# Optimization experiments

Measured on AMD Instinct MI355X. Metric: run time of the kernel, lower is better.

## Reference

```python
import jax, jax.numpy as jnp
import numpy as np

N_NODES = 100000
N_EDGES = 1600000
IN_DIM = 128
HID = 128
NUM_LAYERS = 3


def _sage_conv(h, src, dst, Wl, Wr, b, n_nodes):
    # PyG SAGEConv (aggr='mean'): out = lin_l(mean_j x_j) + lin_r(x_i)
    agg = jax.ops.segment_sum(h[src], dst, num_segments=n_nodes)
    cnt = jax.ops.segment_sum(jnp.ones((src.shape[0],), dtype=h.dtype), dst,
                              num_segments=n_nodes)
    mean = agg / jnp.maximum(cnt, 1.0)[:, None]
    return mean @ Wl + h @ Wr + b


def setup_inputs() -> dict:
    key = jax.random.key(0)
    ks = jax.random.split(key, 16)
    x = jax.random.normal(ks[0], (N_NODES, IN_DIM), dtype=jnp.float32)
    edge_index = jax.random.randint(ks[1], (2, N_EDGES), 0, N_NODES, dtype=jnp.int32)
    reranker_scores = jax.random.normal(ks[2], (N_NODES,), dtype=jnp.float32)
    inp = {"x": x, "edge_index": edge_index, "reranker_scores": reranker_scores}
    dims = [IN_DIM, HID, HID]
    for i in range(NUM_LAYERS):
        d_in = dims[i]
        s = 1.0 / np.sqrt(d_in)
        inp[f"Wl{i}"] = jax.random.uniform(ks[3 + 3 * i], (d_in, HID), jnp.float32, -s, s)
        inp[f"Wr{i}"] = jax.random.uniform(ks[4 + 3 * i], (d_in, HID), jnp.float32, -s, s)
        inp[f"b{i}"] = jax.random.uniform(ks[5 + 3 * i], (HID,), jnp.float32, -s, s)
    sh = 1.0 / np.sqrt(HID * NUM_LAYERS)
    inp["Ws"] = jax.random.uniform(ks[12], (HID * NUM_LAYERS, 1), jnp.float32, -sh, sh)
    inp["bs"] = jax.random.uniform(ks[13], (1,), jnp.float32, -sh, sh)
    inp["alpha"] = jnp.asarray(0.65, dtype=jnp.float32)
    return inp


def reference(x, edge_index, reranker_scores,
              Wl0, Wr0, b0, Wl1, Wr1, b1, Wl2, Wr2, b2,
              Ws, bs, alpha):
    src, dst = edge_index[0], edge_index[1]
    n = x.shape[0]
    params = [(Wl0, Wr0, b0), (Wl1, Wr1, b1), (Wl2, Wr2, b2)]
    xs = []
    h = x
    for (Wl, Wr, b) in params:
        h = jax.nn.relu(_sage_conv(h, src, dst, Wl, Wr, b, n))
        # dropout: eval-mode identity
        xs.append(h)
    hj = jnp.concatenate(xs, axis=-1)                 # [N, HID*NUM_LAYERS]
    gnn_scores = (hj @ Ws + bs)[:, 0]                 # [N]
    a = jax.nn.sigmoid(alpha)
    return a * reranker_scores + (1.0 - a) * gnn_scores
```

## Files before the change

### kernel.cpp

```cpp
#include <hip/hip_runtime.h>
#include <hip/hip_bf16.h>
#include <cstdint>

#define N_NODES 100000
#define HID 128
#define NBINS 391
#define CHUNK 4096

typedef __attribute__((ext_vector_type(8))) short short8v;
typedef __attribute__((ext_vector_type(4))) float floatx4;

__device__ __forceinline__ float bflo(unsigned v) { return __uint_as_float(v << 16); }
__device__ __forceinline__ float bfhi(unsigned v) { return __uint_as_float(v & 0xffff0000u); }
__device__ __forceinline__ unsigned short f2bf(float f) {
    unsigned u = __float_as_uint(f);
    unsigned r = (u + 0x7fffu + ((u >> 16) & 1u)) >> 16;
    return (unsigned short)r;
}

__global__ __launch_bounds__(256) void prep_kernel(const float* __restrict__ x,
                                                   unsigned short* __restrict__ xb, int total8,
                                                   const float* __restrict__ Wl0, const float* __restrict__ Wr0,
                                                   const float* __restrict__ Wl1, const float* __restrict__ Wr1,
                                                   const float* __restrict__ Wl2, const float* __restrict__ Wr2,
                                                   unsigned short* __restrict__ Bp) {
    if ((int)blockIdx.x < total8 / 256) {
        int i = blockIdx.x * 256 + threadIdx.x;
        const float4* p = (const float4*)x + (size_t)i * 2;
        float4 a = p[0], b = p[1];
        uint4 o;
        o.x = f2bf(a.x) | ((unsigned)f2bf(a.y) << 16);
        o.y = f2bf(a.z) | ((unsigned)f2bf(a.w) << 16);
        o.z = f2bf(b.x) | ((unsigned)f2bf(b.y) << 16);
        o.w = f2bf(b.z) | ((unsigned)f2bf(b.w) << 16);
        *(uint4*)(xb + (size_t)i * 8) = o;
    } else {
        int idx = ((int)blockIdx.x - total8 / 256) * 256 + threadIdx.x;
        if (idx >= 12288) return;
        int g = idx & 3, c = (idx >> 2) & 127, s = (idx >> 9) & 3, t = (idx >> 11) & 1, L = idx >> 12;
        const float* W = (t == 0) ? (L == 0 ? Wl0 : (L == 1 ? Wl1 : Wl2))
                                  : (L == 0 ? Wr0 : (L == 1 ? Wr1 : Wr2));
        int k0 = s * 32 + g * 8;
        uint4 o;
        o.x = f2bf(W[(k0 + 0) * 128 + c]) | ((unsigned)f2bf(W[(k0 + 1) * 128 + c]) << 16);
        o.y = f2bf(W[(k0 + 2) * 128 + c]) | ((unsigned)f2bf(W[(k0 + 3) * 128 + c]) << 16);
        o.z = f2bf(W[(k0 + 4) * 128 + c]) | ((unsigned)f2bf(W[(k0 + 5) * 128 + c]) << 16);
        o.w = f2bf(W[(k0 + 6) * 128 + c]) | ((unsigned)f2bf(W[(k0 + 7) * 128 + c]) << 16);
        size_t chunk = (((size_t)(L * 2 + t) * 4 + s) * 128 + c) * 4 + g;
        *(uint4*)(Bp + chunk * 8) = o;
    }
}


__global__ __launch_bounds__(256) void binhist_kernel(const int* __restrict__ dst,
                                                      int* __restrict__ cntMat, int E) {
    __shared__ int lcnt[512];
    const int tid = threadIdx.x;
    lcnt[tid] = 0; lcnt[tid + 256] = 0;
    __syncthreads();
    int base = blockIdx.x * CHUNK;
    int end = base + CHUNK; if (end > E) end = E;
    for (int i = base + tid; i < end; i += 256) atomicAdd(&lcnt[dst[i] >> 8], 1);
    __syncthreads();
    for (int j = tid; j < NBINS; j += 256) cntMat[(size_t)blockIdx.x * NBINS + j] = lcnt[j];
}

__global__ __launch_bounds__(512) void colscan_kernel(int* __restrict__ cntMat,
                                                      int* __restrict__ binCnt, int nch) {
    __shared__ int wsum[8];
    const int j = blockIdx.x;
    const int tid = threadIdx.x;
    const int lane = tid & 63, w = tid >> 6;
    int v = (tid < nch) ? cntMat[(size_t)tid * NBINS + j] : 0;
    int s = v;
    #pragma unroll
    for (int o = 1; o < 64; o <<= 1) {
        int t = __shfl_up(s, o, 64);
        if (lane >= o) s += t;
    }
    if (lane == 63) wsum[w] = s;
    __syncthreads();
    if (w == 0 && lane < 8) {
        int t = wsum[lane];
        int ss = t;
        #pragma unroll
        for (int o = 1; o < 8; o <<= 1) {
            int u = __shfl_up(ss, o, 64);
            if (lane >= o) ss += u;
        }
        wsum[lane] = ss - t;
    }
    __syncthreads();
    int excl = (s - v) + wsum[w];
    if (tid < nch) cntMat[(size_t)tid * NBINS + j] = excl;
    if (tid == 511) binCnt[j] = excl + v;
}

__global__ __launch_bounds__(512) void binbase_kernel(const int* __restrict__ binCnt,
                                                      int* __restrict__ binBase,
                                                      int* __restrict__ offs, int E) {
    __shared__ int wsum[8];
    const int tid = threadIdx.x;
    const int lane = tid & 63, w = tid >> 6;
    int v = (tid < NBINS) ? binCnt[tid] : 0;
    int s = v;
    #pragma unroll
    for (int o = 1; o < 64; o <<= 1) {
        int t = __shfl_up(s, o, 64);
        if (lane >= o) s += t;
    }
    if (lane == 63) wsum[w] = s;
    __syncthreads();
    if (w == 0 && lane < 8) {
        int t = wsum[lane];
        int ss = t;
        #pragma unroll
        for (int o = 1; o < 8; o <<= 1) {
            int u = __shfl_up(ss, o, 64);
            if (lane >= o) ss += u;
        }
        wsum[lane] = ss - t;
    }
    __syncthreads();
    if (tid < NBINS) binBase[tid] = (s - v) + wsum[w];
    if (tid == 0) offs[N_NODES] = E;
}

__global__ __launch_bounds__(256) void binscat_kernel(const int* __restrict__ src, const int* __restrict__ dst,
                                                      const int* __restrict__ cntMat,
                                                      const int* __restrict__ binBase,
                                                      unsigned* __restrict__ binned, int E) {
    __shared__ int cur[512];
    const int tid = threadIdx.x;
    const int row = blockIdx.x;
    for (int j = tid; j < NBINS; j += 256) cur[j] = cntMat[(size_t)row * NBINS + j] + binBase[j];
    __syncthreads();
    int base = row * CHUNK;
    int end = base + CHUNK; if (end > E) end = E;
    for (int i = base + tid; i < end; i += 256) {
        int d = dst[i];
        int s = src[i];
        int bin = d >> 8;
        int pos = atomicAdd(&cur[bin], 1);
        binned[pos] = (unsigned)s | ((unsigned)(d & 255) << 20);
    }
}

__global__ __launch_bounds__(256) void bincsr_kernel(const unsigned* __restrict__ binned,
                                                     const int* __restrict__ binBase, const int* __restrict__ binCnt,
                                                     int* __restrict__ esrc, int* __restrict__ offs) {
    __shared__ int h[256];
    __shared__ int cur[256];
    __shared__ int ssrc[8192];
    const int tid = threadIdx.x;
    const int bin = blockIdx.x;
    const int base = binBase[bin];
    const int cnt = binCnt[bin];
    h[tid] = 0;
    __syncthreads();
    for (int i = tid; i < cnt; i += 256) atomicAdd(&h[binned[base + i] >> 20], 1);
    __syncthreads();
    int v = h[tid];
    for (int o = 1; o < 256; o <<= 1) {
        int t = (tid >= o) ? h[tid - o] : 0;
        __syncthreads();
        h[tid] += t;
        __syncthreads();
    }
    int excl = h[tid] - v;
    cur[tid] = excl;
    int node = (bin << 8) + tid;
    if (node < N_NODES) offs[node] = base + excl;
    __syncthreads();
    for (int i = tid; i < cnt; i += 256) {
        unsigned p = binned[base + i];
        int pos = atomicAdd(&cur[p >> 20], 1);
        int s = (int)(p & 0xFFFFFu);
        if (pos < 8192) ssrc[pos] = s;
        else esrc[base + pos] = s;
    }
    __syncthreads();
    int lim = cnt < 8192 ? cnt : 8192;
    for (int i = tid; i < lim; i += 256) esrc[base + i] = ssrc[i];
}

__global__ __launch_bounds__(256) void agg_kernel(const unsigned short* __restrict__ h,
                                                  const int* __restrict__ offs,
                                                  const int* __restrict__ esrc,
                                                  unsigned short* __restrict__ mean) {
    const int lane = threadIdx.x & 63;
    const int node = blockIdx.x * 4 + (threadIdx.x >> 6);
    const int half = lane >> 5;
    const int fl = lane & 31;
    const int beg = offs[node], end = offs[node + 1];
    const int nb = end - beg;
    float a0 = 0.f, a1 = 0.f, a2 = 0.f, a3 = 0.f;
    for (int base = 0; base < nb; base += 64) {
        int m = nb - base; if (m > 64) m = 64;
        int sv = (lane < m) ? esrc[beg + base + lane] : 0;
        int j = 0;
        for (; j + 16 <= m; j += 16) {
            uint2 v[8];
            #pragma unroll
            for (int p = 0; p < 8; ++p) {
                int s = __shfl(sv, j + 2 * p + half, 64);
                v[p] = *(const uint2*)(h + (size_t)s * HID + fl * 4);
            }
            #pragma unroll
            for (int p = 0; p < 8; ++p) {
                a0 += bflo(v[p].x); a1 += bfhi(v[p].x);
                a2 += bflo(v[p].y); a3 += bfhi(v[p].y);
            }
        }
        for (; j + 2 <= m; j += 2) {
            int s = __shfl(sv, j + half, 64);
            uint2 vv = *(const uint2*)(h + (size_t)s * HID + fl * 4);
            a0 += bflo(vv.x); a1 += bfhi(vv.x);
            a2 += bflo(vv.y); a3 += bfhi(vv.y);
        }
        if (j < m) {
            int s = __shfl(sv, j, 64);
            if (half == 0) {
                uint2 vv = *(const uint2*)(h + (size_t)s * HID + fl * 4);
                a0 += bflo(vv.x); a1 += bfhi(vv.x);
                a2 += bflo(vv.y); a3 += bfhi(vv.y);
            }
        }
    }
    a0 += __shfl_xor(a0, 32, 64);
    a1 += __shfl_xor(a1, 32, 64);
    a2 += __shfl_xor(a2, 32, 64);
    a3 += __shfl_xor(a3, 32, 64);
    if (half == 0) {
        float inv = 1.f / (float)(nb > 0 ? nb : 1);
        uint2 o;
        o.x = (unsigned)f2bf(a0 * inv) | ((unsigned)f2bf(a1 * inv) << 16);
        o.y = (unsigned)f2bf(a2 * inv) | ((unsigned)f2bf(a3 * inv) << 16);
        *(uint2*)(mean + (size_t)node * HID + fl * 4) = o;
    }
}

__global__ __launch_bounds__(256) void gemm_kernel(const unsigned short* __restrict__ Am,
                                                   const unsigned short* __restrict__ Ah,
                                                   const unsigned short* __restrict__ Bp,
                                                   const float* __restrict__ bias,
                                                   const float* __restrict__ Wsl,
                                                   unsigned short* __restrict__ hout,
                                                   float* __restrict__ score,
                                                   const float* __restrict__ rrs,
                                                   const float* __restrict__ bsp,
                                                   const float* __restrict__ alphap,
                                                   float* __restrict__ outF,
                                                   const int accum, const int writeH, const int doFinal) {
    __shared__ unsigned short At[2 * 64 * 128];
    __shared__ float sred[2][64];
    const int tid = threadIdx.x;
    const int lane = tid & 63;
    const int w = tid >> 6;
    const int wm = w & 1, wn = w >> 1;
    const int rowBase = blockIdx.x * 64;
    const int halfRow = lane & 15;
    const int g = lane >> 4;

    {
        const unsigned short* srcs[2] = { Am, Ah };
        #pragma unroll
        for (int r = 0; r < 8; ++r) {
            int c = r * 256 + tid;
            int sIdx = c >> 10;
            int rem = c & 1023;
            int row = rem >> 4, slot = rem & 15;
            int gslot = slot ^ (row & 15);
            int grow = rowBase + row; if (grow >= N_NODES) grow = N_NODES - 1;
            const unsigned short* gp = srcs[sIdx] + (size_t)grow * HID + gslot * 8;
            unsigned ldsOff = (unsigned)(r * 4096 + w * 1024);
            __builtin_amdgcn_global_load_lds((const __attribute__((address_space(1))) void*)gp,
                                             (__attribute__((address_space(3))) void*)((char*)At + ldsOff),
                                             16, 0, 0);
        }
    }
    __syncthreads();

    floatx4 acc[2][4];
    #pragma unroll
    for (int m = 0; m < 2; m++)
        #pragma unroll
        for (int n = 0; n < 4; n++) acc[m][n] = (floatx4){0.f, 0.f, 0.f, 0.f};

    #pragma unroll
    for (int t = 0; t < 2; t++) {
        #pragma unroll
        for (int s = 0; s < 4; s++) {
            int slot = (s * 4 + g) ^ halfRow;
            int row0 = wm * 32 + halfRow;
            short8v a0 = *(const short8v*)&At[t * 8192 + row0 * 128 + slot * 8];
            short8v a1 = *(const short8v*)&At[t * 8192 + (row0 + 16) * 128 + slot * 8];
            #pragma unroll
            for (int n = 0; n < 4; n++) {
                int col = wn * 64 + n * 16 + halfRow;
                short8v b = *(const short8v*)&Bp[((((size_t)(t * 4 + s)) * 128 + col) * 4 + g) * 8];
                acc[0][n] = __builtin_amdgcn_mfma_f32_16x16x32_bf16(a0, b, acc[0][n], 0, 0, 0);
                acc[1][n] = __builtin_amdgcn_mfma_f32_16x16x32_bf16(a1, b, acc[1][n], 0, 0, 0);
            }
        }
    }

    #pragma unroll
    for (int m = 0; m < 2; m++) {
        #pragma unroll
        for (int i = 0; i < 4; i++) {
            int rloc = wm * 32 + m * 16 + g * 4 + i;
            int grow = rowBase + rloc;
            float ps = 0.f;
            #pragma unroll
            for (int n = 0; n < 4; n++) {
                int col = wn * 64 + n * 16 + halfRow;
                float v = acc[m][n][i] + bias[col];
                v = fmaxf(v, 0.f);
                if (writeH && grow < N_NODES) hout[(size_t)grow * HID + col] = f2bf(v);
                ps += v * Wsl[col];
            }
            ps += __shfl_xor(ps, 1, 64);
            ps += __shfl_xor(ps, 2, 64);
            ps += __shfl_xor(ps, 4, 64);
            ps += __shfl_xor(ps, 8, 64);
            if (halfRow == 0) sred[wn][rloc] = ps;
        }
    }
    __syncthreads();
    if (w == 0) {
        int grow = rowBase + lane;
        if (grow < N_NODES) {
            float tot = sred[0][lane] + sred[1][lane];
            if (doFinal) {
                float sc = score[grow] + tot;
                float a = 1.f / (1.f + __expf(-alphap[0]));
                outF[grow] = a * rrs[grow] + (1.f - a) * (sc + bsp[0]);
            } else {
                score[grow] = accum ? (score[grow] + tot) : tot;
            }
        }
    }
}

extern "C" void kernel_launch(void* const* d_in, const int* in_sizes, int n_in,
                              void* d_out, int out_size, void* d_ws, size_t ws_size,
                              hipStream_t stream) {
    const float* x     = (const float*)d_in[0];
    const int*   eidx  = (const int*)d_in[1];
    const float* rrs   = (const float*)d_in[2];
    const float* Wl0   = (const float*)d_in[3];
    const float* Wr0   = (const float*)d_in[4];
    const float* b0    = (const float*)d_in[5];
    const float* Wl1   = (const float*)d_in[6];
    const float* Wr1   = (const float*)d_in[7];
    const float* b1    = (const float*)d_in[8];
    const float* Wl2   = (const float*)d_in[9];
    const float* Wr2   = (const float*)d_in[10];
    const float* b2    = (const float*)d_in[11];
    const float* Ws    = (const float*)d_in[12];
    const float* bs    = (const float*)d_in[13];
    const float* alpha = (const float*)d_in[14];

    const int N = N_NODES;
    const int E = in_sizes[1] / 2;
    const int* src = eidx;
    const int* dst = eidx + E;

    uintptr_t p = (uintptr_t)d_ws;
    auto alloc = [&](size_t bytes) -> void* {
        p = (p + 255) & ~(uintptr_t)255;
        void* r = (void*)p;
        p += bytes;
        return r;
    };
    int*            offs    = (int*)alloc((size_t)(N + 1) * 4);
    int*            esrc    = (int*)alloc((size_t)E * 4);
    float*          score   = (float*)alloc((size_t)N * 4);
    int*            binBase = (int*)alloc(512 * 4);
    int*            binCnt  = (int*)alloc(512 * 4);
    unsigned short* xb      = (unsigned short*)alloc((size_t)N * HID * 2);
    unsigned short* bufA    = (unsigned short*)alloc((size_t)N * HID * 2);
    unsigned short* bufB    = (unsigned short*)alloc((size_t)N * HID * 2);
    unsigned short* Bp      = (unsigned short*)alloc((size_t)3 * 32768 * 2);

    int*      cntMat = (int*)bufA;
    unsigned* binned = (unsigned*)bufB;

    const int nch = (E + CHUNK - 1) / CHUNK;

    prep_kernel<<<N * HID / 8 / 256 + 48, 256, 0, stream>>>(x, xb, N * HID / 8,
                                                            Wl0, Wr0, Wl1, Wr1, Wl2, Wr2, Bp);

    binhist_kernel<<<nch, 256, 0, stream>>>(dst, cntMat, E);
    colscan_kernel<<<NBINS, 512, 0, stream>>>(cntMat, binCnt, nch);
    binbase_kernel<<<1, 512, 0, stream>>>(binCnt, binBase, offs, E);
    binscat_kernel<<<nch, 256, 0, stream>>>(src, dst, cntMat, binBase, binned, E);
    bincsr_kernel<<<NBINS, 256, 0, stream>>>(binned, binBase, binCnt, esrc, offs);

    const int aggGrid  = N / 4;
    const int gemmGrid = (N + 63) / 64;
    float* outF = (float*)d_out;

    agg_kernel<<<aggGrid, 256, 0, stream>>>(xb, offs, esrc, bufA);
    gemm_kernel<<<gemmGrid, 256, 0, stream>>>(bufA, xb, Bp + 0 * 32768, b0, Ws + 0 * HID, bufA, score,
                                              rrs, bs, alpha, outF, 0, 1, 0);
    agg_kernel<<<aggGrid, 256, 0, stream>>>(bufA, offs, esrc, bufB);
    gemm_kernel<<<gemmGrid, 256, 0, stream>>>(bufB, bufA, Bp + 1 * 32768, b1, Ws + 1 * HID, bufB, score,
                                              rrs, bs, alpha, outF, 1, 1, 0);
    agg_kernel<<<aggGrid, 256, 0, stream>>>(bufB, offs, esrc, bufA);
    gemm_kernel<<<gemmGrid, 256, 0, stream>>>(bufA, bufB, Bp + 2 * 32768, b2, Ws + 2 * HID, bufA, score,
                                              rrs, bs, alpha, outF, 1, 0, 1);
}
```

Baseline: 318.0 us.

## Fuse neighbor mean aggregation into the per-layer GEMM kernel via LDS

Merges the separate aggregation and GEMM kernels into one kernel per layer. Each block gathers the mean of neighbour features for its 64 rows straight into swizzled shared memory while the self features stream in asynchronously, then runs the MFMA GEMM. This removes writing and re-reading the intermediate mean buffer and cuts the launches from six to three. In exchange, grid parallelism for the gather drops (1563 blocks of 64 nodes instead of 25000 blocks of 4), and each wave processes 16 nodes one after another, which may reduce latency hiding.

Result: slower. 401.7 us (+26.3%).

```diff
diff --git a/kernel.cpp b/kernel.cpp
--- a/kernel.cpp
+++ b/kernel.cpp
@@ -184,102 +184,100 @@
     for (int i = tid; i < lim; i += 256) esrc[base + i] = ssrc[i];
 }
 
-__global__ __launch_bounds__(256) void agg_kernel(const unsigned short* __restrict__ h,
-                                                  const int* __restrict__ offs,
-                                                  const int* __restrict__ esrc,
-                                                  unsigned short* __restrict__ mean) {
-    const int lane = threadIdx.x & 63;
-    const int node = blockIdx.x * 4 + (threadIdx.x >> 6);
+__global__ __launch_bounds__(256) void fused_kernel(const unsigned short* __restrict__ hin,
+                                                    const int* __restrict__ offs,
+                                                    const int* __restrict__ esrc,
+                                                    const unsigned short* __restrict__ Bp,
+                                                    const float* __restrict__ bias,
+                                                    const float* __restrict__ Wsl,
+                                                    unsigned short* __restrict__ hout,
+                                                    float* __restrict__ score,
+                                                    const float* __restrict__ rrs,
+                                                    const float* __restrict__ bsp,
+                                                    const float* __restrict__ alphap,
+                                                    float* __restrict__ outF,
+                                                    const int accum, const int writeH, const int doFinal) {
+    __shared__ unsigned short At[2 * 64 * 128];
+    __shared__ float sred[2][64];
+    const int tid = threadIdx.x;
+    const int lane = tid & 63;
+    const int w = tid >> 6;
+    const int rowBase = blockIdx.x * 64;
+
+    #pragma unroll
+    for (int r = 0; r < 4; ++r) {
+        int c = r * 256 + tid;
+        int row = c >> 4, slot = c & 15;
+        int gslot = slot ^ (row & 15);
+        int grow = rowBase + row; if (grow >= N_NODES) grow = N_NODES - 1;
+        const unsigned short* gp = hin + (size_t)grow * HID + gslot * 8;
+        unsigned ldsOff = 16384u + (unsigned)(r * 4096 + w * 1024);
+        __builtin_amdgcn_global_load_lds((const __attribute__((address_space(1))) void*)gp,
+                                         (__attribute__((address_space(3))) void*)((char*)At + ldsOff),
+                                         16, 0, 0);
+    }
+
     const int half = lane >> 5;
     const int fl = lane & 31;
-    const int beg = offs[node], end = offs[node + 1];
-    const int nb = end - beg;
-    float a0 = 0.f, a1 = 0.f, a2 = 0.f, a3 = 0.f;
-    for (int base = 0; base < nb; base += 64) {
-        int m = nb - base; if (m > 64) m = 64;
-        int sv = (lane < m) ? esrc[beg + base + lane] : 0;
-        int j = 0;
-        for (; j + 16 <= m; j += 16) {
-            uint2 v[8];
-            #pragma unroll
-            for (int p = 0; p < 8; ++p) {
-                int s = __shfl(sv, j + 2 * p + half, 64);
-                v[p] = *(const uint2*)(h + (size_t)s * HID + fl * 4);
+    for (int k = 0; k < 16; ++k) {
+        const int nl = w * 16 + k;
+        const int node = rowBase + nl;
+        float a0 = 0.f, a1 = 0.f, a2 = 0.f, a3 = 0.f;
+        int nb = 0;
+        if (node < N_NODES) {
+            const int beg = offs[node], end = offs[node + 1];
+            nb = end - beg;
+            for (int base = 0; base < nb; base += 64) {
+                int m = nb - base; if (m > 64) m = 64;
+                int sv = (lane < m) ? esrc[beg + base + lane] : 0;
+                int j = 0;
+                for (; j + 16 <= m; j += 16) {
+                    uint2 v[8];
+                    #pragma unroll
+                    for (int p = 0; p < 8; ++p) {
+                        int s = __shfl(sv, j + 2 * p + half, 64);
+                        v[p] = *(const uint2*)(hin + (size_t)s * HID + fl * 4);
+                    }
+                    #pragma unroll
+                    for (int p = 0; p < 8; ++p) {
+                        a0 += bflo(v[p].x); a1 += bfhi(v[p].x);
+                        a2 += bflo(v[p].y); a3 += bfhi(v[p].y);
+                    }
+                }
+                for (; j + 2 <= m; j += 2) {
+                    int s = __shfl(sv, j + half, 64);
+                    uint2 vv = *(const uint2*)(hin + (size_t)s * HID + fl * 4);
+                    a0 += bflo(vv.x); a1 += bfhi(vv.x);
+                    a2 += bflo(vv.y); a3 += bfhi(vv.y);
+                }
+                if (j < m) {
+                    int s = __shfl(sv, j, 64);
+                    if (half == 0) {
+                        uint2 vv = *(const uint2*)(hin + (size_t)s * HID + fl * 4);
+                        a0 += bflo(vv.x); a1 += bfhi(vv.x);
+                        a2 += bflo(vv.y); a3 += bfhi(vv.y);
+                    }
+                }
             }
-            #pragma unroll
-            for (int p = 0; p < 8; ++p) {
-                a0 += bflo(v[p].x); a1 += bfhi(v[p].x);
-                a2 += bflo(v[p].y); a3 += bfhi(v[p].y);
-            }
-        }
-        for (; j + 2 <= m; j += 2) {
-            int s = __shfl(sv, j + half, 64);
-            uint2 vv = *(const uint2*)(h + (size_t)s * HID + fl * 4);
-            a0 += bflo(vv.x); a1 += bfhi(vv.x);
-            a2 += bflo(vv.y); a3 += bfhi(vv.y);
-        }
-        if (j < m) {
-            int s = __shfl(sv, j, 64);
-            if (half == 0) {
-                uint2 vv = *(const uint2*)(h + (size_t)s * HID + fl * 4);
-                a0 += bflo(vv.x); a1 += bfhi(vv.x);
-                a2 += bflo(vv.y); a3 += bfhi(vv.y);
-            }
-        }
-    }
-    a0 += __shfl_xor(a0, 32, 64);
-    a1 += __shfl_xor(a1, 32, 64);
-    a2 += __shfl_xor(a2, 32, 64);
-    a3 += __shfl_xor(a3, 32, 64);
-    if (half == 0) {
-        float inv = 1.f / (float)(nb > 0 ? nb : 1);
-        uint2 o;
-        o.x = (unsigned)f2bf(a0 * inv) | ((unsigned)f2bf(a1 * inv) << 16);
-        o.y = (unsigned)f2bf(a2 * inv) | ((unsigned)f2bf(a3 * inv) << 16);
-        *(uint2*)(mean + (size_t)node * HID + fl * 4) = o;
-    }
-}
-
-__global__ __launch_bounds__(256) void gemm_kernel(const unsigned short* __restrict__ Am,
-                                                   const unsigned short* __restrict__ Ah,
-                                                   const unsigned short* __restrict__ Bp,
-                                                   const float* __restrict__ bias,
-                                                   const float* __restrict__ Wsl,
-                                                   unsigned short* __restrict__ hout,
-                                                   float* __restrict__ score,
-                                                   const float* __restrict__ rrs,
-                                                   const float* __restrict__ bsp,
-                                                   const float* __restrict__ alphap,
-                                                   float* __restrict__ outF,
-                                                   const int accum, const int writeH, const int doFinal) {
-    __shared__ unsigned short At[2 * 64 * 128];
-    __shared__ float sred[2][64];
-    const int tid = threadIdx.x;
-    const int lane = tid & 63;
-    const int w = tid >> 6;
+        }
+        a0 += __shfl_xor(a0, 32, 64);
+        a1 += __shfl_xor(a1, 32, 64);
+        a2 += __shfl_xor(a2, 32, 64);
+        a3 += __shfl_xor(a3, 32, 64);
+        if (half == 0) {
+            float inv = 1.f / (float)(nb > 0 ? nb : 1);
+            uint2 o;
+            o.x = (unsigned)f2bf(a0 * inv) | ((unsigned)f2bf(a1 * inv) << 16);
+            o.y = (unsigned)f2bf(a2 * inv) | ((unsigned)f2bf(a3 * inv) << 16);
+            int sw = (fl >> 1) ^ (nl & 15);
+            *(uint2*)&At[nl * 128 + sw * 8 + (fl & 1) * 4] = o;
+        }
+    }
+    __syncthreads();
+
     const int wm = w & 1, wn = w >> 1;
-    const int rowBase = blockIdx.x * 64;
     const int halfRow = lane & 15;
     const int g = lane >> 4;
-
-    {
-        const unsigned short* srcs[2] = { Am, Ah };
-        #pragma unroll
-        for (int r = 0; r < 8; ++r) {
-            int c = r * 256 + tid;
-            int sIdx = c >> 10;
-            int rem = c & 1023;
-            int row = rem >> 4, slot = rem & 15;
-            int gslot = slot ^ (row & 15);
-            int grow = rowBase + row; if (grow >= N_NODES) grow = N_NODES - 1;
-            const unsigned short* gp = srcs[sIdx] + (size_t)grow * HID + gslot * 8;
-            unsigned ldsOff = (unsigned)(r * 4096 + w * 1024);
-            __builtin_amdgcn_global_load_lds((const __attribute__((address_space(1))) void*)gp,
-                                             (__attribute__((address_space(3))) void*)((char*)At + ldsOff),
-                                             16, 0, 0);
-        }
-    }
-    __syncthreads();
 
     floatx4 acc[2][4];
     #pragma unroll
@@ -398,17 +396,13 @@
     binscat_kernel<<<nch, 256, 0, stream>>>(src, dst, cntMat, binBase, binned, E);
     bincsr_kernel<<<NBINS, 256, 0, stream>>>(binned, binBase, binCnt, esrc, offs);
 
-    const int aggGrid  = N / 4;
     const int gemmGrid = (N + 63) / 64;
     float* outF = (float*)d_out;
 
-    agg_kernel<<<aggGrid, 256, 0, stream>>>(xb, offs, esrc, bufA);
-    gemm_kernel<<<gemmGrid, 256, 0, stream>>>(bufA, xb, Bp + 0 * 32768, b0, Ws + 0 * HID, bufA, score,
-                                              rrs, bs, alpha, outF, 0, 1, 0);
-    agg_kernel<<<aggGrid, 256, 0, stream>>>(bufA, offs, esrc, bufB);
-    gemm_kernel<<<gemmGrid, 256, 0, stream>>>(bufB, bufA, Bp + 1 * 32768, b1, Ws + 1 * HID, bufB, score,
-                                              rrs, bs, alpha, outF, 1, 1, 0);
-    agg_kernel<<<aggGrid, 256, 0, stream>>>(bufB, offs, esrc, bufA);
-    gemm_kernel<<<gemmGrid, 256, 0, stream>>>(bufA, bufB, Bp + 2 * 32768, b2, Ws + 2 * HID, bufA, score,
-                                              rrs, bs, alpha, outF, 1, 0, 1);
-}
+    fused_kernel<<<gemmGrid, 256, 0, stream>>>(xb, offs, esrc, Bp + 0 * 32768, b0, Ws + 0 * HID,
+                                               bufA, score, rrs, bs, alpha, outF, 0, 1, 0);
+    fused_kernel<<<gemmGrid, 256, 0, stream>>>(bufA, offs, esrc, Bp + 1 * 32768, b1, Ws + 1 * HID,
+                                               bufB, score, rrs, bs, alpha, outF, 1, 1, 0);
+    fused_kernel<<<gemmGrid, 256, 0, stream>>>(bufB, offs, esrc, Bp + 2 * 32768, b2, Ws + 2 * HID,
+                                               bufB, score, rrs, bs, alpha, outF, 1, 0, 1);
+}
```
